# Performance work log

Hardware: AMD Instinct MI355X
Metric: run time of the kernel (lower is better)

Reference implementation:

```python
import jax, jax.numpy as jnp
import numpy as np

N_NODES = 100000
N_EDGES = 3200000
IN_FEATS = 16
OUT_FEATS = 2
K = 3


def setup_inputs() -> dict:
    key = jax.random.key(0)
    k1, k2, k3, k4 = jax.random.split(key, 4)
    in_feat = jax.random.normal(k1, (N_NODES, IN_FEATS), dtype=jnp.float32)
    # Linear(K*in_feats -> out_feats, bias=False) weight, torch layout (out, in)
    W = jax.random.normal(k2, (OUT_FEATS, K * IN_FEATS), dtype=jnp.float32) * (1.0 / np.sqrt(K * IN_FEATS))
    src = jax.random.randint(k3, (N_EDGES,), 0, N_NODES, dtype=jnp.int64)
    dst = jax.random.randint(k4, (N_EDGES,), 0, N_NODES, dtype=jnp.int64)
    # cached dgl.laplacian_lambda_max value; 2.0 is the normalized-Laplacian bound
    lambda_max = jnp.full((1,), 2.0, dtype=jnp.float32)
    return {"in_feat": in_feat, "W": W, "src": src, "dst": dst, "lambda_max": lambda_max}


def reference(in_feat, W, src, dst, lambda_max):
    N = in_feat.shape[0]
    # in-degree based symmetric normalization, clamp(min=1)
    deg = jax.ops.segment_sum(jnp.ones_like(dst, dtype=in_feat.dtype), dst, num_segments=N)
    norm = jnp.clip(deg, 1.0) ** -0.5  # (N,)
    norm = norm[:, None]
    re_norm = (2.0 / lambda_max)[None, :]  # (1,1), broadcasts over nodes

    def prop(x):
        # D^{-1/2} A D^{-1/2} x via gather from src, scatter-sum to dst
        m = (x * norm)[src]                                    # (E, d)
        return jax.ops.segment_sum(m, dst, num_segments=N) * norm

    X0 = in_feat
    X1 = -re_norm * prop(X0) + X0 * (re_norm - 1.0)
    X2 = -2.0 * re_norm * prop(X1) + X1 * (2.0 * (re_norm - 1.0)) - X0
    Xt = jnp.concatenate([X0, X1, X2], axis=1)                 # (N, K*d)
    h = Xt @ W.T                                               # (N, out)
    return jax.nn.relu(h)  # DGL ChebConv default activation
```

## Files before the change

kernel.cpp:

```cpp
#include <hip/hip_runtime.h>
#include <hip/hip_bf16.h>


#define NN   100000
#define NE   3200000
#define F    16
#define CB   128
#define NBUK 782
#define ECHK 8192
#define NBLK 391
#define LCAP 5632
#define HXW  1025
#define PCAP 4608

__device__ __forceinline__ float bflo(unsigned int u) {
    return __uint_as_float(u << 16);
}
__device__ __forceinline__ float bfhi(unsigned int u) {
    return __uint_as_float(u & 0xffff0000u);
}
__device__ __forceinline__ unsigned int f2bf(float f) {
    __hip_bfloat16 b = __float2bfloat16(f);
    return (unsigned int)*reinterpret_cast<unsigned short*>(&b);
}

__global__ __launch_bounds__(512) void k_lsort(const int* __restrict__ src,
        const int* __restrict__ dst, int* __restrict__ hxg, int* __restrict__ csort) {
    __shared__ __align__(16) int pk[ECHK];
    __shared__ int hx[HXW];
    __shared__ int cur[1024];
    __shared__ int csum[512];
    int t = threadIdx.x, blk = blockIdx.x;
    for (int j = t; j < 1024; j += 512) hx[j] = 0;
    __syncthreads();
    int s0 = blk * ECHK;
    int lim = min(s0 + ECHK, NE);
    int n4 = (lim - s0) >> 2;
    const int4* dst4 = (const int4*)(dst + s0);
    const int4* src4 = (const int4*)(src + s0);
    for (int i = t; i < n4; i += 512) {
        int4 d = dst4[i];
        atomicAdd(&hx[d.x >> 7], 1);
        atomicAdd(&hx[d.y >> 7], 1);
        atomicAdd(&hx[d.z >> 7], 1);
        atomicAdd(&hx[d.w >> 7], 1);
    }
    __syncthreads();
    int b0 = t * 2;
    int c0 = hx[b0], c1 = hx[b0 + 1];
    csum[t] = c0 + c1;
    __syncthreads();
    for (int o = 1; o < 512; o <<= 1) {
        int add = (t >= o) ? csum[t - o] : 0;
        __syncthreads();
        csum[t] += add;
        __syncthreads();
    }
    int ce = csum[t] - (c0 + c1);
    hx[b0] = ce;  hx[b0 + 1] = ce + c0;
    cur[b0] = ce; cur[b0 + 1] = ce + c0;
    if (t == 511) hx[1024] = csum[511];
    __syncthreads();
    for (int j = t; j < HXW; j += 512)
        hxg[blk * HXW + j] = hx[j];
    for (int i = t; i < n4; i += 512) {
        int4 d = dst4[i];
        int4 s = src4[i];
        int pos;
        pos = atomicAdd(&cur[d.x >> 7], 1); pk[pos] = (s.x << 7) | (d.x & 127);
        pos = atomicAdd(&cur[d.y >> 7], 1); pk[pos] = (s.y << 7) | (d.y & 127);
        pos = atomicAdd(&cur[d.z >> 7], 1); pk[pos] = (s.z << 7) | (d.z & 127);
        pos = atomicAdd(&cur[d.w >> 7], 1); pk[pos] = (s.w << 7) | (d.w & 127);
    }
    __syncthreads();
    int4* cs4 = (int4*)(csort + s0);
    const int4* pk4 = (const int4*)pk;
    for (int i = t; i < n4; i += 512)
        cs4[i] = pk4[i];
}

__global__ __launch_bounds__(512) void k_sort(const int* __restrict__ csort,
        const int* __restrict__ hxg, const float* __restrict__ X0,
        int* __restrict__ es, unsigned int* __restrict__ P,
        unsigned short* __restrict__ Y0, unsigned short* __restrict__ Y1) {
    __shared__ __align__(16) int pk[LCAP];
    __shared__ __align__(16) int pk2[LCAP];
    __shared__ int dsc[512];
    __shared__ int hS[NBLK];
    __shared__ short rls[NBLK];
    __shared__ int cnt[CB], loc[CB], cur[CB];
    __shared__ float nvs[CB];
    int b = blockIdx.x, t = threadIdx.x;
    int h0 = 0, rl = 0;
    if (t < NBLK) {
        h0 = hxg[t * HXW + b];
        rl = hxg[t * HXW + b + 1] - h0;
        hS[t] = h0;
        rls[t] = (short)(rl > 4096 ? 4096 : rl);
    }
    dsc[t] = rl;
    if (t < CB) cnt[t] = 0;
    if (b == 0 && t < 4) {
        ((uint2*)Y0)[(size_t)NN * 4 + t] = make_uint2(0u, 0u);
        ((uint2*)Y1)[(size_t)NN * 4 + t] = make_uint2(0u, 0u);
    }
    __syncthreads();
    for (int o = 1; o < 512; o <<= 1) {
        int add = (t >= o) ? dsc[t - o] : 0;
        __syncthreads();
        dsc[t] += add;
        __syncthreads();
    }
    int len = dsc[511];
    if (len > LCAP) len = LCAP;
    int g = t >> 4, lane = t & 15;
    for (int c = g; c < NBLK; c += 32) {
        int rlc = rls[c];
        if (rlc == 0) continue;
        int dpos = dsc[c] - rlc;
        if (dpos >= LCAP) continue;
        if (dpos + rlc > LCAP) rlc = LCAP - dpos;
        int sb = c * ECHK + hS[c];
        for (int l = lane; l < rlc; l += 16)
            pk[dpos + l] = csort[sb + l];
    }
    __syncthreads();
    for (int i = t; i < len; i += 512)
        atomicAdd(&cnt[pk[i] & 127], 1);
    __syncthreads();
    int pc = 0;
    if (t < CB) { pc = (cnt[t] + 7) & ~7; loc[t] = pc; }
    __syncthreads();
    for (int o = 1; o < CB; o <<= 1) {
        int add = 0;
        if (t < CB && t >= o) add = loc[t - o];
        __syncthreads();
        if (t < CB) loc[t] += add;
        __syncthreads();
    }
    if (t < CB) {
        int excl = loc[t] - pc;
        loc[t] = excl;
        cur[t] = excl;
        int n = b * CB + t;
        if (n < NN) {
            unsigned dgc = cnt[t] > 1023 ? 1023u : (unsigned)cnt[t];
            P[n] = ((unsigned)((b * LCAP + excl) >> 3) << 10) | dgc;
            nvs[t] = rsqrtf((float)(cnt[t] < 1 ? 1 : cnt[t]));
        }
    }
    __syncthreads();
    int plen = loc[CB - 1] + ((cnt[CB - 1] + 7) & ~7);
    if (plen > LCAP) plen = LCAP;
    if (t < CB) {
        int e0 = loc[t] + cnt[t];
        int e1 = loc[t] + ((cnt[t] + 7) & ~7);
        for (int i = e0; i < e1 && i < LCAP; ++i) pk2[i] = NN;
    }
    for (int i = t; i < len; i += 512) {
        int p = pk[i];
        int pos = atomicAdd(&cur[p & 127], 1);
        if (pos < LCAP) pk2[pos] = p >> 7;
    }
    for (int j = t; j < CB * 4; j += 512) {
        int dl = j >> 2;
        int n = b * CB + dl;
        if (n < NN) {
            float nv = nvs[dl];
            size_t g4 = (size_t)n * 4 + (j & 3);
            float4 x0 = ((const float4*)X0)[g4];
            uint2 o;
            o.x = f2bf(x0.x * nv) | (f2bf(x0.y * nv) << 16);
            o.y = f2bf(x0.z * nv) | (f2bf(x0.w * nv) << 16);
            ((uint2*)Y0)[g4] = o;
        }
    }
    __syncthreads();
    int4* es4 = (int4*)(es + b * LCAP);
    const int4* p24 = (const int4*)pk2;
    int p4 = plen >> 2;
    for (int i = t; i < p4; i += 512)
        es4[i] = p24[i];
}

__global__ __launch_bounds__(256) void k_prop1(const unsigned int* __restrict__ P,
        const int* __restrict__ es, const unsigned short* __restrict__ Y0,
        const float* __restrict__ X0, const float* __restrict__ lm,
        unsigned short* __restrict__ Y1) {
    __shared__ __align__(16) int sidx[PCAP];
    int blk = blockIdx.x, t = threadIdx.x;
    int b = blk >> 1, half = blk & 1;
    int n0 = b * CB + half * 64;
    if (n0 >= NN) return;
    unsigned pk0 = P[n0];
    int nL = min(n0 + 63, NN - 1);
    unsigned pkL = P[nL];
    int st = (int)(pk0 >> 10) << 3;
    int en = ((int)(pkL >> 10) << 3) + (int)(((pkL & 1023u) + 7u) & ~7u);
    int slen = en - st;
    if (slen > PCAP) slen = PCAP;
    const int4* esg = (const int4*)(es + st);
    int4* sid4 = (int4*)sidx;
    int s4 = slen >> 2;
    for (int i = t; i < s4; i += 256)
        sid4[i] = esg[i];
    __syncthreads();
    int n = n0 + (t >> 2), h = t & 3;
    if (n >= NN) return;
    unsigned pkn = P[n];
    int beg = ((int)(pkn >> 10) << 3) - st;
    int dg = (int)(pkn & 1023u);
    int nb = (dg + 7) >> 3;
    const uint2* Yv = (const uint2*)Y0;
    float a0 = 0.f, a1 = 0.f, a2 = 0.f, a3 = 0.f;
    for (int bb = 0; bb < nb; ++bb) {
        int e0 = beg + bb * 8;
        int4 ia = *(const int4*)&sidx[e0];
        int4 ib = *(const int4*)&sidx[e0 + 4];
#define ACC(S) { uint2 u = Yv[(size_t)(S) * 4 + h]; \
                 a0 += bflo(u.x); a1 += bfhi(u.x); \
                 a2 += bflo(u.y); a3 += bfhi(u.y); }
        ACC(ia.x) ACC(ia.y) ACC(ia.z) ACC(ia.w)
        ACC(ib.x) ACC(ib.y) ACC(ib.z) ACC(ib.w)
    }
    float nv = rsqrtf((float)(dg < 1 ? 1 : dg));
    float r  = 2.0f / lm[0];
    float k1 = -r * nv, k2 = r - 1.0f;
    int tid4 = n * 4 + h;
    float4 x0 = ((const float4*)X0)[tid4];
    float x1a = k1 * a0 + k2 * x0.x;
    float x1b = k1 * a1 + k2 * x0.y;
    float x1c = k1 * a2 + k2 * x0.z;
    float x1d = k1 * a3 + k2 * x0.w;
    uint2 o;
    o.x = f2bf(nv * x1a) | (f2bf(nv * x1b) << 16);
    o.y = f2bf(nv * x1c) | (f2bf(nv * x1d) << 16);
    ((uint2*)Y1)[tid4] = o;
}

__global__ __launch_bounds__(256) void k_prop2(const unsigned int* __restrict__ P,
        const int* __restrict__ es, const unsigned short* __restrict__ Y1,
        const float* __restrict__ X0, const float* __restrict__ lm,
        const float* __restrict__ W, float* __restrict__ out) {
    __shared__ __align__(16) int sidx[PCAP];
    __shared__ float Ws[96];
    int blk = blockIdx.x, t = threadIdx.x;
    int b = blk >> 1, half = blk & 1;
    int n0 = b * CB + half * 64;
    if (n0 >= NN) return;
    if (t < 96) Ws[t] = W[t];
    unsigned pk0 = P[n0];
    int nL = min(n0 + 63, NN - 1);
    unsigned pkL = P[nL];
    int st = (int)(pk0 >> 10) << 3;
    int en = ((int)(pkL >> 10) << 3) + (int)(((pkL & 1023u) + 7u) & ~7u);
    int slen = en - st;
    if (slen > PCAP) slen = PCAP;
    const int4* esg = (const int4*)(es + st);
    int4* sid4 = (int4*)sidx;
    int s4 = slen >> 2;
    for (int i = t; i < s4; i += 256)
        sid4[i] = esg[i];
    __syncthreads();
    int n = n0 + (t >> 2), h = t & 3;
    if (n >= NN) return;
    unsigned pkn = P[n];
    int beg = ((int)(pkn >> 10) << 3) - st;
    int dg = (int)(pkn & 1023u);
    int nb = (dg + 7) >> 3;
    const uint2* Yv = (const uint2*)Y1;
    float a0 = 0.f, a1 = 0.f, a2 = 0.f, a3 = 0.f;
    for (int bb = 0; bb < nb; ++bb) {
        int e0 = beg + bb * 8;
        int4 ia = *(const int4*)&sidx[e0];
        int4 ib = *(const int4*)&sidx[e0 + 4];
        ACC(ia.x) ACC(ia.y) ACC(ia.z) ACC(ia.w)
        ACC(ib.x) ACC(ib.y) ACC(ib.z) ACC(ib.w)
    }
    int dc = dg < 1 ? 1 : dg;
    float nv = rsqrtf((float)dc);
    float rn = sqrtf((float)dc);
    float r  = 2.0f / lm[0];
    int tid4 = n * 4 + h;
    float4 x0 = ((const float4*)X0)[tid4];
    uint2 uy = ((const uint2*)Y1)[tid4];
    float x1a = bflo(uy.x) * rn, x1b = bfhi(uy.x) * rn;
    float x1c = bflo(uy.y) * rn, x1d = bfhi(uy.y) * rn;
    float c1 = -2.0f * r * nv, c2 = 2.0f * (r - 1.0f);
    float x2a = c1 * a0 + c2 * x1a - x0.x;
    float x2b = c1 * a1 + c2 * x1b - x0.y;
    float x2c = c1 * a2 + c2 * x1c - x0.z;
    float x2d = c1 * a3 + c2 * x1d - x0.w;
    int f0 = 4 * h;
    float t0 = Ws[f0] * x0.x + Ws[f0 + 1] * x0.y + Ws[f0 + 2] * x0.z + Ws[f0 + 3] * x0.w
             + Ws[16 + f0] * x1a + Ws[17 + f0] * x1b + Ws[18 + f0] * x1c + Ws[19 + f0] * x1d
             + Ws[32 + f0] * x2a + Ws[33 + f0] * x2b + Ws[34 + f0] * x2c + Ws[35 + f0] * x2d;
    float t1 = Ws[48 + f0] * x0.x + Ws[49 + f0] * x0.y + Ws[50 + f0] * x0.z + Ws[51 + f0] * x0.w
             + Ws[64 + f0] * x1a + Ws[65 + f0] * x1b + Ws[66 + f0] * x1c + Ws[67 + f0] * x1d
             + Ws[80 + f0] * x2a + Ws[81 + f0] * x2b + Ws[82 + f0] * x2c + Ws[83 + f0] * x2d;
    t0 += __shfl_xor(t0, 2, 4); t0 += __shfl_xor(t0, 1, 4);
    t1 += __shfl_xor(t1, 2, 4); t1 += __shfl_xor(t1, 1, 4);
    if (h == 0) {
        out[(size_t)n * 2 + 0] = fmaxf(t0, 0.f);
        out[(size_t)n * 2 + 1] = fmaxf(t1, 0.f);
    }
}

extern "C" void kernel_launch(void* const* d_in, const int* in_sizes, int n_in,
                              void* d_out, int out_size, void* d_ws, size_t ws_size,
                              hipStream_t stream) {
    const float* X0  = (const float*)d_in[0];
    const float* W   = (const float*)d_in[1];
    const int*   src = (const int*)d_in[2];
    const int*   dst = (const int*)d_in[3];
    const float* lm  = (const float*)d_in[4];
    float* out = (float*)d_out;

    int*   hxg   = (int*)d_ws;
    int*   csort = hxg + (size_t)NBLK * HXW;
    int*   es    = csort + NE;
    unsigned int* P = (unsigned int*)(es + (size_t)NBUK * LCAP);
    unsigned short* Y0 = (unsigned short*)(P + NN);
    unsigned short* Y1 = Y0 + (size_t)(NN + 1) * F;

    k_lsort<<<NBLK, 512, 0, stream>>>(src, dst, hxg, csort);
    k_sort <<<NBUK, 512, 0, stream>>>(csort, hxg, X0, es, P, Y0, Y1);
    k_prop1<<<NBUK * 2, 256, 0, stream>>>(P, es, Y0, X0, lm, Y1);
    k_prop2<<<NBUK * 2, 256, 0, stream>>>(P, es, Y1, X0, lm, W, out);
}
```

Measured before the change: 161.5 us.

## Register-cache edge chunks, use wave-shuffle scans, drop LDS staging in propagation

In the local sort kernel, each thread now keeps its src/dst int4 loads in registers between the histogram pass and the scatter pass, so global memory is read only once. The sort kernel's barrier-heavy shared-memory prefix scans are replaced with wavefront shuffle scans plus a small cross-wave combine, cutting the number of __syncthreads. Both propagation kernels stop staging edge indices into LDS and read them directly from global memory as int4. Their grid becomes one block per 64 nodes, which removes the LDS footprint and the block barrier but relies on L1/L2 caching for the index reads.

```diff
diff --git a/kernel.cpp b/kernel.cpp
--- a/kernel.cpp
+++ b/kernel.cpp
@@ -11,7 +11,6 @@
 #define NBLK 391
 #define LCAP 5632
 #define HXW  1025
-#define PCAP 4608
 
 __device__ __forceinline__ float bflo(unsigned int u) {
     return __uint_as_float(u << 16);
@@ -38,12 +37,19 @@
     int n4 = (lim - s0) >> 2;
     const int4* dst4 = (const int4*)(dst + s0);
     const int4* src4 = (const int4*)(src + s0);
-    for (int i = t; i < n4; i += 512) {
-        int4 d = dst4[i];
-        atomicAdd(&hx[d.x >> 7], 1);
-        atomicAdd(&hx[d.y >> 7], 1);
-        atomicAdd(&hx[d.z >> 7], 1);
-        atomicAdd(&hx[d.w >> 7], 1);
+    int4 dreg[4], sreg[4];
+#pragma unroll
+    for (int k = 0; k < 4; ++k) {
+        int i = t + (k << 9);
+        if (i < n4) {
+            int4 d = dst4[i];
+            int4 s = src4[i];
+            dreg[k] = d; sreg[k] = s;
+            atomicAdd(&hx[d.x >> 7], 1);
+            atomicAdd(&hx[d.y >> 7], 1);
+            atomicAdd(&hx[d.z >> 7], 1);
+            atomicAdd(&hx[d.w >> 7], 1);
+        }
     }
     __syncthreads();
     int b0 = t * 2;
@@ -63,14 +69,18 @@
     __syncthreads();
     for (int j = t; j < HXW; j += 512)
         hxg[blk * HXW + j] = hx[j];
-    for (int i = t; i < n4; i += 512) {
-        int4 d = dst4[i];
-        int4 s = src4[i];
-        int pos;
-        pos = atomicAdd(&cur[d.x >> 7], 1); pk[pos] = (s.x << 7) | (d.x & 127);
-        pos = atomicAdd(&cur[d.y >> 7], 1); pk[pos] = (s.y << 7) | (d.y & 127);
-        pos = atomicAdd(&cur[d.z >> 7], 1); pk[pos] = (s.z << 7) | (d.z & 127);
-        pos = atomicAdd(&cur[d.w >> 7], 1); pk[pos] = (s.w << 7) | (d.w & 127);
+#pragma unroll
+    for (int k = 0; k < 4; ++k) {
+        int i = t + (k << 9);
+        if (i < n4) {
+            int4 d = dreg[k];
+            int4 s = sreg[k];
+            int pos;
+            pos = atomicAdd(&cur[d.x >> 7], 1); pk[pos] = (s.x << 7) | (d.x & 127);
+            pos = atomicAdd(&cur[d.y >> 7], 1); pk[pos] = (s.y << 7) | (d.y & 127);
+            pos = atomicAdd(&cur[d.z >> 7], 1); pk[pos] = (s.z << 7) | (d.z & 127);
+            pos = atomicAdd(&cur[d.w >> 7], 1); pk[pos] = (s.w << 7) | (d.w & 127);
+        }
     }
     __syncthreads();
     int4* cs4 = (int4*)(csort + s0);
@@ -88,9 +98,12 @@
     __shared__ int dsc[512];
     __shared__ int hS[NBLK];
     __shared__ short rls[NBLK];
+    __shared__ int wsum[8];
+    __shared__ int ws2[2];
     __shared__ int cnt[CB], loc[CB], cur[CB];
     __shared__ float nvs[CB];
     int b = blockIdx.x, t = threadIdx.x;
+    int ln = t & 63, wv = t >> 6;
     int h0 = 0, rl = 0;
     if (t < NBLK) {
         h0 = hxg[t * HXW + b];
@@ -98,19 +111,26 @@
         hS[t] = h0;
         rls[t] = (short)(rl > 4096 ? 4096 : rl);
     }
-    dsc[t] = rl;
     if (t < CB) cnt[t] = 0;
     if (b == 0 && t < 4) {
         ((uint2*)Y0)[(size_t)NN * 4 + t] = make_uint2(0u, 0u);
         ((uint2*)Y1)[(size_t)NN * 4 + t] = make_uint2(0u, 0u);
     }
-    __syncthreads();
-    for (int o = 1; o < 512; o <<= 1) {
-        int add = (t >= o) ? dsc[t - o] : 0;
-        __syncthreads();
-        dsc[t] += add;
-        __syncthreads();
-    }
+    int v = rl;
+    for (int o = 1; o < 64; o <<= 1) {
+        int up = __shfl_up(v, o, 64);
+        if (ln >= o) v += up;
+    }
+    if (ln == 63) wsum[wv] = v;
+    __syncthreads();
+    if (t == 0) {
+        int acc = 0;
+        for (int i = 0; i < 8; ++i) { int x = wsum[i]; wsum[i] = acc; acc += x; }
+    }
+    __syncthreads();
+    v += wsum[wv];
+    dsc[t] = v;
+    __syncthreads();
     int len = dsc[511];
     if (len > LCAP) len = LCAP;
     int g = t >> 4, lane = t & 15;
@@ -128,18 +148,17 @@
     for (int i = t; i < len; i += 512)
         atomicAdd(&cnt[pk[i] & 127], 1);
     __syncthreads();
-    int pc = 0;
-    if (t < CB) { pc = (cnt[t] + 7) & ~7; loc[t] = pc; }
-    __syncthreads();
-    for (int o = 1; o < CB; o <<= 1) {
-        int add = 0;
-        if (t < CB && t >= o) add = loc[t - o];
-        __syncthreads();
-        if (t < CB) loc[t] += add;
-        __syncthreads();
-    }
+    int pc = 0, vv = 0;
+    if (t < CB) { pc = (cnt[t] + 7) & ~7; vv = pc; }
+    for (int o = 1; o < 64; o <<= 1) {
+        int up = __shfl_up(vv, o, 64);
+        if (ln >= o) vv += up;
+    }
+    if (t < CB && ln == 63) ws2[wv] = vv;
+    __syncthreads();
     if (t < CB) {
-        int excl = loc[t] - pc;
+        if (wv == 1) vv += ws2[0];
+        int excl = vv - pc;
         loc[t] = excl;
         cur[t] = excl;
         int n = b * CB + t;
@@ -187,36 +206,19 @@
         const int* __restrict__ es, const unsigned short* __restrict__ Y0,
         const float* __restrict__ X0, const float* __restrict__ lm,
         unsigned short* __restrict__ Y1) {
-    __shared__ __align__(16) int sidx[PCAP];
-    int blk = blockIdx.x, t = threadIdx.x;
-    int b = blk >> 1, half = blk & 1;
-    int n0 = b * CB + half * 64;
-    if (n0 >= NN) return;
-    unsigned pk0 = P[n0];
-    int nL = min(n0 + 63, NN - 1);
-    unsigned pkL = P[nL];
-    int st = (int)(pk0 >> 10) << 3;
-    int en = ((int)(pkL >> 10) << 3) + (int)(((pkL & 1023u) + 7u) & ~7u);
-    int slen = en - st;
-    if (slen > PCAP) slen = PCAP;
-    const int4* esg = (const int4*)(es + st);
-    int4* sid4 = (int4*)sidx;
-    int s4 = slen >> 2;
-    for (int i = t; i < s4; i += 256)
-        sid4[i] = esg[i];
-    __syncthreads();
-    int n = n0 + (t >> 2), h = t & 3;
+    int t = threadIdx.x;
+    int n = blockIdx.x * 64 + (t >> 2), h = t & 3;
     if (n >= NN) return;
     unsigned pkn = P[n];
-    int beg = ((int)(pkn >> 10) << 3) - st;
+    int begq = (int)(pkn >> 10) << 1;
     int dg = (int)(pkn & 1023u);
     int nb = (dg + 7) >> 3;
+    const int4* esq = (const int4*)es;
     const uint2* Yv = (const uint2*)Y0;
     float a0 = 0.f, a1 = 0.f, a2 = 0.f, a3 = 0.f;
     for (int bb = 0; bb < nb; ++bb) {
-        int e0 = beg + bb * 8;
-        int4 ia = *(const int4*)&sidx[e0];
-        int4 ib = *(const int4*)&sidx[e0 + 4];
+        int4 ia = esq[begq + bb * 2];
+        int4 ib = esq[begq + bb * 2 + 1];
 #define ACC(S) { uint2 u = Yv[(size_t)(S) * 4 + h]; \
                  a0 += bflo(u.x); a1 += bfhi(u.x); \
                  a2 += bflo(u.y); a3 += bfhi(u.y); }
@@ -242,38 +244,22 @@
         const int* __restrict__ es, const unsigned short* __restrict__ Y1,
         const float* __restrict__ X0, const float* __restrict__ lm,
         const float* __restrict__ W, float* __restrict__ out) {
-    __shared__ __align__(16) int sidx[PCAP];
     __shared__ float Ws[96];
-    int blk = blockIdx.x, t = threadIdx.x;
-    int b = blk >> 1, half = blk & 1;
-    int n0 = b * CB + half * 64;
-    if (n0 >= NN) return;
+    int t = threadIdx.x;
     if (t < 96) Ws[t] = W[t];
-    unsigned pk0 = P[n0];
-    int nL = min(n0 + 63, NN - 1);
-    unsigned pkL = P[nL];
-    int st = (int)(pk0 >> 10) << 3;
-    int en = ((int)(pkL >> 10) << 3) + (int)(((pkL & 1023u) + 7u) & ~7u);
-    int slen = en - st;
-    if (slen > PCAP) slen = PCAP;
-    const int4* esg = (const int4*)(es + st);
-    int4* sid4 = (int4*)sidx;
-    int s4 = slen >> 2;
-    for (int i = t; i < s4; i += 256)
-        sid4[i] = esg[i];
-    __syncthreads();
-    int n = n0 + (t >> 2), h = t & 3;
+    __syncthreads();
+    int n = blockIdx.x * 64 + (t >> 2), h = t & 3;
     if (n >= NN) return;
     unsigned pkn = P[n];
-    int beg = ((int)(pkn >> 10) << 3) - st;
+    int begq = (int)(pkn >> 10) << 1;
     int dg = (int)(pkn & 1023u);
     int nb = (dg + 7) >> 3;
+    const int4* esq = (const int4*)es;
     const uint2* Yv = (const uint2*)Y1;
     float a0 = 0.f, a1 = 0.f, a2 = 0.f, a3 = 0.f;
     for (int bb = 0; bb < nb; ++bb) {
-        int e0 = beg + bb * 8;
-        int4 ia = *(const int4*)&sidx[e0];
-        int4 ib = *(const int4*)&sidx[e0 + 4];
+        int4 ia = esq[begq + bb * 2];
+        int4 ib = esq[begq + bb * 2 + 1];
         ACC(ia.x) ACC(ia.y) ACC(ia.z) ACC(ia.w)
         ACC(ib.x) ACC(ib.y) ACC(ib.z) ACC(ib.w)
     }
@@ -323,8 +309,10 @@
     unsigned short* Y0 = (unsigned short*)(P + NN);
     unsigned short* Y1 = Y0 + (size_t)(NN + 1) * F;
 
+    const int gridP = (NN + 63) / 64;
+
     k_lsort<<<NBLK, 512, 0, stream>>>(src, dst, hxg, csort);
     k_sort <<<NBUK, 512, 0, stream>>>(csort, hxg, X0, es, P, Y0, Y1);
-    k_prop1<<<NBUK * 2, 256, 0, stream>>>(P, es, Y0, X0, lm, Y1);
-    k_prop2<<<NBUK * 2, 256, 0, stream>>>(P, es, Y1, X0, lm, W, out);
-}
+    k_prop1<<<gridP, 256, 0, stream>>>(P, es, Y0, X0, lm, Y1);
+    k_prop2<<<gridP, 256, 0, stream>>>(P, es, Y1, X0, lm, W, out);
+}
```

After: 170.2 us. 5.4% more time.
